# Optimization experiments

Measured on AMD Instinct MI355X. Metric: run time of the kernel, lower is better.

Reference implementation:

```python
import jax, jax.numpy as jnp
import numpy as np

N, K, D = 32768, 32, 64
LOG_2PI = float(np.log(2.0 * np.pi))


def setup_inputs() -> dict:
    key = jax.random.key(0)
    k1, k2, k3, k4 = jax.random.split(key, 4)
    X = jax.random.normal(k1, (N, D), dtype=jnp.float32)
    mu = jax.random.normal(k2, (K, D), dtype=jnp.float32)
    L = jax.random.normal(k3, (K, D, D), dtype=jnp.float32) * 0.1
    weights = jax.random.normal(k4, (K,), dtype=jnp.float32)
    return {"X": X, "mu": mu, "L": L, "weights": weights, "it": 0}


def reference(X, mu, L, weights, it):
    d = X.shape[1]
    # Cholesky composition: Sigma_k = tril(L_k) @ tril(L_k).T + I  (always PD)
    Lt = jnp.tril(L)                                   # [K, D, D]
    sigmas = Lt @ jnp.swapaxes(Lt, -1, -2) + jnp.eye(d, dtype=X.dtype)
    _, logdet = jnp.linalg.slogdet(sigmas)             # [K] (det > 0, sign = +1)
    Sinv = jnp.linalg.inv(sigmas)                      # [K, D, D]
    # Batched squared Mahalanobis distance: [N, K]
    diff = X[:, None, :] - mu[None, :, :]              # [N, K, D]
    maha = jnp.einsum("nkd,kde,nke->nk", diff, Sinv, diff)
    log_w = jax.nn.log_softmax(weights)                # [K]
    # log component density + log mixture weight
    logp = -0.5 * (d * LOG_2PI + logdet[None, :] + maha) + log_w[None, :]
    # pdf = sum_k exp(logp); log_likelihood = log(pdf)  (stable via logsumexp)
    loglik = jax.scipy.special.logsumexp(logp, axis=1)  # [N]
    # forward = -log_likelihoods(X).logsumexp(dim=0)
    return -jax.scipy.special.logsumexp(loglik, axis=0)
```

## Files before the change

### kernel.cpp

```cpp
#include <hip/hip_runtime.h>
#include <math.h>

#define DIM 64
#define KC 32
#define NPTS 32768
#define LOG_2PI 1.8378770664093453f
#define C0 (-58.0f)
#define ST 68

typedef __attribute__((ext_vector_type(8))) short short8;
typedef __attribute__((ext_vector_type(4))) float float4v;

__device__ __forceinline__ unsigned short f2bf(float f) {
    unsigned u = __float_as_uint(f);
    u += 0x7FFFu + ((u >> 16) & 1u);
    return (unsigned short)(u >> 16);
}

__device__ __forceinline__ float rdlane(float v, int l) {
    return __int_as_float(__builtin_amdgcn_readlane(__float_as_int(v), l));
}

template <int CTRL>
__device__ __forceinline__ float dpp_add(float x) {
    int t = __builtin_amdgcn_mov_dpp(__float_as_int(x), CTRL, 0xF, 0xF, true);
    return x + __int_as_float(t);
}
__device__ __forceinline__ float sum16(float x) {
    x = dpp_add<0xB1>(x);
    x = dpp_add<0x4E>(x);
    x = dpp_add<0x141>(x);
    x = dpp_add<0x140>(x);
    return x;
}

__global__ __launch_bounds__(256) void prep_kernel(
    const float* __restrict__ L, const float* __restrict__ mu,
    const float* __restrict__ w, short* __restrict__ Bpack,
    float* __restrict__ cstC)
{
    const int k = blockIdx.x;
    const int t = threadIdx.x;
    const int wv = t >> 6;
    const int ln = t & 63;
    __shared__ float Llds[DIM * ST];
    __shared__ float Sig[DIM * ST];
    __shared__ float Clds[DIM * ST];
    __shared__ float Ylds[DIM * ST];
    __shared__ float qlds[DIM];
    __shared__ float rdbuf[DIM];
    __shared__ float ldet;

    for (int idx = t; idx < DIM * DIM; idx += 256) {
        int r = idx >> 6, c = idx & 63;
        float v = L[(size_t)k * DIM * DIM + idx];
        Llds[r * ST + c] = (c <= r) ? v : 0.f;
    }
    for (int idx = t; idx < DIM * ST; idx += 256) {
        Clds[idx] = 0.f;
        Ylds[idx] = 0.f;
    }
    __syncthreads();

    {
        float Lr[DIM];
        const float2* lp = (const float2*)(Llds + ln * ST);
#pragma unroll
        for (int p = 0; p < 32; ++p) {
            float2 v = lp[p];
            Lr[2 * p] = v.x; Lr[2 * p + 1] = v.y;
        }
#pragma unroll 1
        for (int jj = 0; jj < 16; ++jj) {
            const int j = wv * 16 + jj;
            const float2* up = (const float2*)(Llds + j * ST);
            float a0 = 0.f, a1 = 0.f, a2 = 0.f, a3 = 0.f;
#pragma unroll
            for (int p = 0; p < 32; p += 2) {
                float2 u0 = up[p], u1 = up[p + 1];
                a0 = fmaf(Lr[2 * p], u0.x, a0);
                a1 = fmaf(Lr[2 * p + 1], u0.y, a1);
                a2 = fmaf(Lr[2 * p + 2], u1.x, a2);
                a3 = fmaf(Lr[2 * p + 3], u1.y, a3);
            }
            float s = (a0 + a1) + (a2 + a3);
            if (j == ln) s += 1.f;
            Sig[ln * ST + j] = s;
        }
    }
    __syncthreads();

    {
        const float2* crow = (const float2*)(Clds + ln * ST);
        const float2* yrow = (const float2*)(Ylds + ln * ST);
        float ld2 = 0.f;
#pragma unroll 1
        for (int c = 0; c < DIM; c += 4) {
            const float2* u0 = (const float2*)(Clds + (c + 0) * ST);
            const float2* u1 = (const float2*)(Clds + (c + 1) * ST);
            const float2* u2 = (const float2*)(Clds + (c + 2) * ST);
            const float2* u3 = (const float2*)(Clds + (c + 3) * ST);
            float si0 = 0.f, si1 = 0.f, si2 = 0.f, si3 = 0.f;
            if (wv == 0) {
                float d0a = 0.f, d0b = 0.f, d1a = 0.f, d1b = 0.f;
                float d2a = 0.f, d2b = 0.f, d3a = 0.f, d3b = 0.f;
#pragma unroll
                for (int p = 0; p < 32; ++p) {
                    float2 cr = crow[p];
                    float2 a0 = u0[p], a1 = u1[p], a2 = u2[p], a3 = u3[p];
                    d0a = fmaf(cr.x, a0.x, d0a); d0b = fmaf(cr.y, a0.y, d0b);
                    d1a = fmaf(cr.x, a1.x, d1a); d1b = fmaf(cr.y, a1.y, d1b);
                    d2a = fmaf(cr.x, a2.x, d2a); d2b = fmaf(cr.y, a2.y, d2b);
                    d3a = fmaf(cr.x, a3.x, d3a); d3b = fmaf(cr.y, a3.y, d3b);
                }
                const float4 sg = *(const float4*)(Sig + ln * ST + c);
                float s0 = sg.x - (d0a + d0b);
                float s1 = sg.y - (d1a + d1b);
                float s2 = sg.z - (d2a + d2b);
                float s3 = sg.w - (d3a + d3b);
                float dd0 = rdlane(s0, c + 0);
                float rd0 = __builtin_amdgcn_rsqf(dd0);
                float c0v = s0 * rd0;
                s1 = fmaf(-c0v, rdlane(c0v, c + 1), s1);
                s2 = fmaf(-c0v, rdlane(c0v, c + 2), s2);
                s3 = fmaf(-c0v, rdlane(c0v, c + 3), s3);
                float dd1 = rdlane(s1, c + 1);
                float rd1 = __builtin_amdgcn_rsqf(dd1);
                float c1v = s1 * rd1;
                s2 = fmaf(-c1v, rdlane(c1v, c + 2), s2);
                s3 = fmaf(-c1v, rdlane(c1v, c + 3), s3);
                float dd2 = rdlane(s2, c + 2);
                float rd2 = __builtin_amdgcn_rsqf(dd2);
                float c2v = s2 * rd2;
                s3 = fmaf(-c2v, rdlane(c2v, c + 3), s3);
                float dd3 = rdlane(s3, c + 3);
                float rd3 = __builtin_amdgcn_rsqf(dd3);
                float c3v = s3 * rd3;
                ld2 += (__logf(dd0) + __logf(dd1)) + (__logf(dd2) + __logf(dd3));
                *(float4*)(Clds + ln * ST + c) = make_float4(c0v, c1v, c2v, c3v);
                if (ln == 0) *(float4*)(rdbuf + c) = make_float4(rd0, rd1, rd2, rd3);
            } else if (wv == 1) {
                float e0a = 0.f, e0b = 0.f, e1a = 0.f, e1b = 0.f;
                float e2a = 0.f, e2b = 0.f, e3a = 0.f, e3b = 0.f;
#pragma unroll
                for (int p = 0; p < 32; ++p) {
                    float2 yr = yrow[p];
                    float2 a0 = u0[p], a1 = u1[p], a2 = u2[p], a3 = u3[p];
                    e0a = fmaf(yr.x, a0.x, e0a); e0b = fmaf(yr.y, a0.y, e0b);
                    e1a = fmaf(yr.x, a1.x, e1a); e1b = fmaf(yr.y, a1.y, e1b);
                    e2a = fmaf(yr.x, a2.x, e2a); e2b = fmaf(yr.y, a2.y, e2b);
                    e3a = fmaf(yr.x, a3.x, e3a); e3b = fmaf(yr.y, a3.y, e3b);
                }
                si0 = ((ln == c + 0) ? 1.f : 0.f) - (e0a + e0b);
                si1 = ((ln == c + 1) ? 1.f : 0.f) - (e1a + e1b);
                si2 = ((ln == c + 2) ? 1.f : 0.f) - (e2a + e2b);
                si3 = ((ln == c + 3) ? 1.f : 0.f) - (e3a + e3b);
            }
            __syncthreads();
            if (wv == 1) {
                const float4 rdv = *(const float4*)(rdbuf + c);
                float C10 = Clds[(c + 1) * ST + c];
                float C20 = Clds[(c + 2) * ST + c];
                float C21 = Clds[(c + 2) * ST + c + 1];
                float C30 = Clds[(c + 3) * ST + c];
                float C31 = Clds[(c + 3) * ST + c + 1];
                float C32 = Clds[(c + 3) * ST + c + 2];
                float y0 = si0 * rdv.x;
                float y1 = (si1 - C10 * y0) * rdv.y;
                float y2 = (si2 - C20 * y0 - C21 * y1) * rdv.z;
                float y3 = (si3 - C30 * y0 - C31 * y1 - C32 * y2) * rdv.w;
                float4 yo;
                yo.x = (ln <= c + 0) ? y0 : 0.f;
                yo.y = (ln <= c + 1) ? y1 : 0.f;
                yo.z = (ln <= c + 2) ? y2 : 0.f;
                yo.w = (ln <= c + 3) ? y3 : 0.f;
                *(float4*)(Ylds + ln * ST + c) = yo;
            }
        }
        if (wv == 0 && ln == 0) ldet = ld2;
    }
    __syncthreads();

    if (wv == 0) {
        const float* muk = mu + k * DIM;
        float qv = 0.f;
#pragma unroll 8
        for (int j = 0; j < DIM; ++j)
            qv = fmaf(Ylds[j * ST + ln], muk[j], qv);
        qlds[ln] = qv;
        if (ln == 0) {
            float wm = -3.0e38f;
            for (int i = 0; i < KC; ++i) wm = fmaxf(wm, w[i]);
            float se = 0.f;
            for (int i = 0; i < KC; ++i) se += __expf(w[i] - wm);
            float logw = w[k] - (wm + __logf(se));
            cstC[k] = -0.5f * (DIM * LOG_2PI + ldet) + logw - C0;
        }
    }
    __syncthreads();

    {
        const int ct = wv;
        const int col = ct * 16 + (ln & 15);
        const int kb = (ln >> 4) * 8;
#pragma unroll
        for (int kt = 0; kt < 3; ++kt) {
            short8 v;
            if (kt < 2) {
#pragma unroll
                for (int e = 0; e < 8; ++e)
                    v[e] = (short)f2bf(Ylds[(kt * 32 + kb + e) * ST + col]);
            } else {
#pragma unroll
                for (int e = 0; e < 8; ++e)
                    v[e] = (short)((kb + e == 0) ? f2bf(-qlds[col]) : 0);
            }
            *(short8*)(Bpack + ((size_t)(k * 12 + ct * 3 + kt) * 64 + ln) * 8) = v;
        }
    }
}

__global__ __launch_bounds__(256, 2) void main_kernel(
    const float* __restrict__ X, const float* __restrict__ Bpack,
    const float* __restrict__ cstC, float* __restrict__ partials)
{
    const int tid = threadIdx.x;
    const int lane = tid & 63;
    const int wv = tid >> 6;
    const int ks = blockIdx.x & 7;
    const int g = blockIdx.x >> 3;

    __shared__ float4 Bsh[3072];
    {
        const float4* Bg = (const float4*)Bpack + (size_t)ks * 3072;
#pragma unroll
        for (int it = 0; it < 12; ++it)
            Bsh[it * 256 + tid] = Bg[it * 256 + tid];
    }

    const int rbase = g * 128 + wv * 32;
    const int jb = (lane >> 4) * 8;
    const float* Xr0 = X + (size_t)(rbase + (lane & 15)) * DIM;
    const float* Xr1 = Xr0 + 16 * DIM;
    short8 a0, a1, b0r, b1r;
#pragma unroll
    for (int e = 0; e < 8; ++e) {
        a0[e] = (short)f2bf(Xr0[jb + e]);
        a1[e] = (short)f2bf(Xr0[32 + jb + e]);
        b0r[e] = (short)f2bf(Xr1[jb + e]);
        b1r[e] = (short)f2bf(Xr1[32 + jb + e]);
    }
    short8 a2 = (short8)0;
    if (lane < 16) a2[0] = (short)0x3F80;

    __syncthreads();

    const short8* Bs = (const short8*)Bsh;
    float acc = 0.f;
#pragma unroll
    for (int kk = 0; kk < 4; ++kk) {
        const int k = ks * 4 + kk;
        float p0 = 0.f, p1 = 0.f, p2 = 0.f, p3 = 0.f;
        float r0 = 0.f, r1 = 0.f, r2 = 0.f, r3 = 0.f;
#pragma unroll
        for (int ct = 0; ct < 4; ++ct) {
            short8 f0 = Bs[(kk * 12 + ct * 3 + 0) * 64 + lane];
            short8 f1 = Bs[(kk * 12 + ct * 3 + 1) * 64 + lane];
            short8 f2 = Bs[(kk * 12 + ct * 3 + 2) * 64 + lane];
            float4v c0 = {0.f, 0.f, 0.f, 0.f};
            c0 = __builtin_amdgcn_mfma_f32_16x16x32_bf16(a0, f0, c0, 0, 0, 0);
            c0 = __builtin_amdgcn_mfma_f32_16x16x32_bf16(a1, f1, c0, 0, 0, 0);
            c0 = __builtin_amdgcn_mfma_f32_16x16x32_bf16(a2, f2, c0, 0, 0, 0);
            float4v c1 = {0.f, 0.f, 0.f, 0.f};
            c1 = __builtin_amdgcn_mfma_f32_16x16x32_bf16(b0r, f0, c1, 0, 0, 0);
            c1 = __builtin_amdgcn_mfma_f32_16x16x32_bf16(b1r, f1, c1, 0, 0, 0);
            c1 = __builtin_amdgcn_mfma_f32_16x16x32_bf16(a2, f2, c1, 0, 0, 0);
            p0 = fmaf(c0[0], c0[0], p0); p1 = fmaf(c0[1], c0[1], p1);
            p2 = fmaf(c0[2], c0[2], p2); p3 = fmaf(c0[3], c0[3], p3);
            r0 = fmaf(c1[0], c1[0], r0); r1 = fmaf(c1[1], c1[1], r1);
            r2 = fmaf(c1[2], c1[2], r2); r3 = fmaf(c1[3], c1[3], r3);
        }
        const float cc = cstC[k];
        acc += __expf(fmaf(-0.5f, sum16(p0), cc)) + __expf(fmaf(-0.5f, sum16(p1), cc));
        acc += __expf(fmaf(-0.5f, sum16(p2), cc)) + __expf(fmaf(-0.5f, sum16(p3), cc));
        acc += __expf(fmaf(-0.5f, sum16(r0), cc)) + __expf(fmaf(-0.5f, sum16(r1), cc));
        acc += __expf(fmaf(-0.5f, sum16(r2), cc)) + __expf(fmaf(-0.5f, sum16(r3), cc));
    }
    acc += __shfl_xor(acc, 16, 64);
    acc += __shfl_xor(acc, 32, 64);

    __shared__ float pm[4];
    if (lane == 0) pm[wv] = acc;
    __syncthreads();
    if (tid == 0)
        partials[blockIdx.x] = (pm[0] + pm[1]) + (pm[2] + pm[3]);
}

__global__ __launch_bounds__(256) void final_kernel(
    const float* __restrict__ partials, int n, float* __restrict__ out)
{
    const int tid = threadIdx.x;
    float s = 0.f;
    for (int i = tid; i < n; i += 256) s += partials[i];
#pragma unroll
    for (int m = 1; m <= 32; m <<= 1) s += __shfl_xor(s, m, 64);
    __shared__ float pm[4];
    if ((tid & 63) == 0) pm[tid >> 6] = s;
    __syncthreads();
    if (tid == 0) out[0] = -(C0 + logf((pm[0] + pm[1]) + (pm[2] + pm[3])));
}

extern "C" void kernel_launch(void* const* d_in, const int* in_sizes, int n_in,
                              void* d_out, int out_size, void* d_ws, size_t ws_size,
                              hipStream_t stream) {
    const float* X  = (const float*)d_in[0];
    const float* mu = (const float*)d_in[1];
    const float* L  = (const float*)d_in[2];
    const float* w  = (const float*)d_in[3];

    char* ws = (char*)d_ws;
    short* Bpack = (short*)ws;
    float* cstC  = (float*)(ws + 32 * 12 * 64 * 8 * 2);
    float* parts = cstC + KC;

    prep_kernel<<<KC, 256, 0, stream>>>(L, mu, w, Bpack, cstC);
    main_kernel<<<2048, 256, 0, stream>>>(X, (const float*)Bpack, cstC, parts);
    final_kernel<<<1, 256, 0, stream>>>(parts, 2048, (float*)d_out);
}
```

Measured before the change: 112.7 us.

## Drop constant-offset MFMA, shrink LDS, raise occupancy, fuse final reduction

Removes the third MFMA per tile that applied the -q offset through a one-hot A fragment. The offset is now added as a scalar read from the packed buffer, which cuts LDS use from 48KB to 32KB, and launch bounds are raised to allow 4 blocks per CU. X loads are vectorized as float4. The separate final reduction kernel is replaced by a last-block-done atomic counter inside the main kernel, saving one launch. The trade-offs are an extra global load per tile, added atomic and fence traffic, and the offset now being added in bf16-rounded form after the matmul rather than inside it.

After: 156.0 us. 38.4% more time.

```diff
diff --git a/kernel.cpp b/kernel.cpp
--- a/kernel.cpp
+++ b/kernel.cpp
@@ -37,7 +37,7 @@
 __global__ __launch_bounds__(256) void prep_kernel(
     const float* __restrict__ L, const float* __restrict__ mu,
     const float* __restrict__ w, short* __restrict__ Bpack,
-    float* __restrict__ cstC)
+    float* __restrict__ cstC, int* __restrict__ counter)
 {
     const int k = blockIdx.x;
     const int t = threadIdx.x;
@@ -50,6 +50,8 @@
     __shared__ float qlds[DIM];
     __shared__ float rdbuf[DIM];
     __shared__ float ldet;
+
+    if (k == 0 && t == 0) *counter = 0;
 
     for (int idx = t; idx < DIM * DIM; idx += 256) {
         int r = idx >> 6, c = idx & 63;
@@ -220,9 +222,10 @@
     }
 }
 
-__global__ __launch_bounds__(256, 2) void main_kernel(
-    const float* __restrict__ X, const float* __restrict__ Bpack,
-    const float* __restrict__ cstC, float* __restrict__ partials)
+__global__ __launch_bounds__(256, 4) void main_kernel(
+    const float* __restrict__ X, const short* __restrict__ Bpack,
+    const float* __restrict__ cstC, float* __restrict__ partials,
+    int* __restrict__ counter, float* __restrict__ out)
 {
     const int tid = threadIdx.x;
     const int lane = tid & 63;
@@ -230,29 +233,35 @@
     const int ks = blockIdx.x & 7;
     const int g = blockIdx.x >> 3;
 
-    __shared__ float4 Bsh[3072];
+    __shared__ float4 Bsh[2048];
     {
-        const float4* Bg = (const float4*)Bpack + (size_t)ks * 3072;
-#pragma unroll
-        for (int it = 0; it < 12; ++it)
-            Bsh[it * 256 + tid] = Bg[it * 256 + tid];
-    }
-
+        const float4* Bg = (const float4*)Bpack;
+#pragma unroll
+        for (int it = 0; it < 8; ++it) {
+            int flat = it * 256 + tid;
+            int frag = flat >> 6, l2 = flat & 63;
+            int kk2 = frag >> 3, ct2 = (frag >> 1) & 3, kt2 = frag & 1;
+            Bsh[flat] = Bg[(size_t)(((ks * 4 + kk2) * 12 + ct2 * 3 + kt2) * 64 + l2)];
+        }
+    }
+
+    const int m = lane & 15;
+    const int h8 = lane >> 4;
     const int rbase = g * 128 + wv * 32;
-    const int jb = (lane >> 4) * 8;
-    const float* Xr0 = X + (size_t)(rbase + (lane & 15)) * DIM;
-    const float* Xr1 = Xr0 + 16 * DIM;
-    short8 a0, a1, b0r, b1r;
-#pragma unroll
-    for (int e = 0; e < 8; ++e) {
-        a0[e] = (short)f2bf(Xr0[jb + e]);
-        a1[e] = (short)f2bf(Xr0[32 + jb + e]);
-        b0r[e] = (short)f2bf(Xr1[jb + e]);
-        b1r[e] = (short)f2bf(Xr1[32 + jb + e]);
-    }
-    short8 a2 = (short8)0;
-    if (lane < 16) a2[0] = (short)0x3F80;
-
+    short8 a[2][2];
+#pragma unroll
+    for (int tt = 0; tt < 2; ++tt) {
+        const float4* Xr = (const float4*)(X + (size_t)(rbase + tt * 16 + m) * DIM);
+#pragma unroll
+        for (int hh = 0; hh < 2; ++hh) {
+            float4 v0 = Xr[hh * 8 + h8 * 2];
+            float4 v1 = Xr[hh * 8 + h8 * 2 + 1];
+            a[tt][hh][0] = (short)f2bf(v0.x); a[tt][hh][1] = (short)f2bf(v0.y);
+            a[tt][hh][2] = (short)f2bf(v0.z); a[tt][hh][3] = (short)f2bf(v0.w);
+            a[tt][hh][4] = (short)f2bf(v1.x); a[tt][hh][5] = (short)f2bf(v1.y);
+            a[tt][hh][6] = (short)f2bf(v1.z); a[tt][hh][7] = (short)f2bf(v1.w);
+        }
+    }
     __syncthreads();
 
     const short8* Bs = (const short8*)Bsh;
@@ -264,21 +273,25 @@
         float r0 = 0.f, r1 = 0.f, r2 = 0.f, r3 = 0.f;
 #pragma unroll
         for (int ct = 0; ct < 4; ++ct) {
-            short8 f0 = Bs[(kk * 12 + ct * 3 + 0) * 64 + lane];
-            short8 f1 = Bs[(kk * 12 + ct * 3 + 1) * 64 + lane];
-            short8 f2 = Bs[(kk * 12 + ct * 3 + 2) * 64 + lane];
+            short8 f0 = Bs[(kk * 8 + ct * 2 + 0) * 64 + lane];
+            short8 f1 = Bs[(kk * 8 + ct * 2 + 1) * 64 + lane];
+            short qs = Bpack[((size_t)(k * 12 + ct * 3 + 2) * 64 + m) * 8];
+            float nq = __int_as_float(((int)(unsigned short)qs) << 16);
             float4v c0 = {0.f, 0.f, 0.f, 0.f};
-            c0 = __builtin_amdgcn_mfma_f32_16x16x32_bf16(a0, f0, c0, 0, 0, 0);
-            c0 = __builtin_amdgcn_mfma_f32_16x16x32_bf16(a1, f1, c0, 0, 0, 0);
-            c0 = __builtin_amdgcn_mfma_f32_16x16x32_bf16(a2, f2, c0, 0, 0, 0);
+            c0 = __builtin_amdgcn_mfma_f32_16x16x32_bf16(a[0][0], f0, c0, 0, 0, 0);
+            c0 = __builtin_amdgcn_mfma_f32_16x16x32_bf16(a[0][1], f1, c0, 0, 0, 0);
             float4v c1 = {0.f, 0.f, 0.f, 0.f};
-            c1 = __builtin_amdgcn_mfma_f32_16x16x32_bf16(b0r, f0, c1, 0, 0, 0);
-            c1 = __builtin_amdgcn_mfma_f32_16x16x32_bf16(b1r, f1, c1, 0, 0, 0);
-            c1 = __builtin_amdgcn_mfma_f32_16x16x32_bf16(a2, f2, c1, 0, 0, 0);
-            p0 = fmaf(c0[0], c0[0], p0); p1 = fmaf(c0[1], c0[1], p1);
-            p2 = fmaf(c0[2], c0[2], p2); p3 = fmaf(c0[3], c0[3], p3);
-            r0 = fmaf(c1[0], c1[0], r0); r1 = fmaf(c1[1], c1[1], r1);
-            r2 = fmaf(c1[2], c1[2], r2); r3 = fmaf(c1[3], c1[3], r3);
+            c1 = __builtin_amdgcn_mfma_f32_16x16x32_bf16(a[1][0], f0, c1, 0, 0, 0);
+            c1 = __builtin_amdgcn_mfma_f32_16x16x32_bf16(a[1][1], f1, c1, 0, 0, 0);
+            float d;
+            d = c0[0] + nq; p0 = fmaf(d, d, p0);
+            d = c0[1] + nq; p1 = fmaf(d, d, p1);
+            d = c0[2] + nq; p2 = fmaf(d, d, p2);
+            d = c0[3] + nq; p3 = fmaf(d, d, p3);
+            d = c1[0] + nq; r0 = fmaf(d, d, r0);
+            d = c1[1] + nq; r1 = fmaf(d, d, r1);
+            d = c1[2] + nq; r2 = fmaf(d, d, r2);
+            d = c1[3] + nq; r3 = fmaf(d, d, r3);
         }
         const float cc = cstC[k];
         acc += __expf(fmaf(-0.5f, sum16(p0), cc)) + __expf(fmaf(-0.5f, sum16(p1), cc));
@@ -290,24 +303,25 @@
     acc += __shfl_xor(acc, 32, 64);
 
     __shared__ float pm[4];
+    __shared__ int lastdone;
     if (lane == 0) pm[wv] = acc;
     __syncthreads();
-    if (tid == 0)
+    if (tid == 0) {
         partials[blockIdx.x] = (pm[0] + pm[1]) + (pm[2] + pm[3]);
-}
-
-__global__ __launch_bounds__(256) void final_kernel(
-    const float* __restrict__ partials, int n, float* __restrict__ out)
-{
-    const int tid = threadIdx.x;
-    float s = 0.f;
-    for (int i = tid; i < n; i += 256) s += partials[i];
-#pragma unroll
-    for (int m = 1; m <= 32; m <<= 1) s += __shfl_xor(s, m, 64);
-    __shared__ float pm[4];
-    if ((tid & 63) == 0) pm[tid >> 6] = s;
-    __syncthreads();
-    if (tid == 0) out[0] = -(C0 + logf((pm[0] + pm[1]) + (pm[2] + pm[3])));
+        __threadfence();
+        lastdone = (atomicAdd(counter, 1) == 2047) ? 1 : 0;
+    }
+    __syncthreads();
+    if (lastdone) {
+        __threadfence();
+        float s = 0.f;
+        for (int i = tid; i < 2048; i += 256) s += partials[i];
+#pragma unroll
+        for (int mm = 1; mm <= 32; mm <<= 1) s += __shfl_xor(s, mm, 64);
+        if (lane == 0) pm[wv] = s;
+        __syncthreads();
+        if (tid == 0) out[0] = -(C0 + logf((pm[0] + pm[1]) + (pm[2] + pm[3])));
+    }
 }
 
 extern "C" void kernel_launch(void* const* d_in, const int* in_sizes, int n_in,
@@ -319,11 +333,11 @@
     const float* w  = (const float*)d_in[3];
 
     char* ws = (char*)d_ws;
-    short* Bpack = (short*)ws;
-    float* cstC  = (float*)(ws + 32 * 12 * 64 * 8 * 2);
-    float* parts = cstC + KC;
-
-    prep_kernel<<<KC, 256, 0, stream>>>(L, mu, w, Bpack, cstC);
-    main_kernel<<<2048, 256, 0, stream>>>(X, (const float*)Bpack, cstC, parts);
-    final_kernel<<<1, 256, 0, stream>>>(parts, 2048, (float*)d_out);
-}
+    short* Bpack   = (short*)ws;
+    float* cstC    = (float*)(ws + 32 * 12 * 64 * 8 * 2);
+    float* parts   = cstC + KC;
+    int*   counter = (int*)(parts + 2048);
+
+    prep_kernel<<<KC, 256, 0, stream>>>(L, mu, w, Bpack, cstC, counter);
+    main_kernel<<<2048, 256, 0, stream>>>(X, Bpack, cstC, parts, counter, (float*)d_out);
+}
```
